# Kernel tuning notes

Measured on AMD Instinct MI355X. Metric: run time of the kernel, lower is better.

Reference implementation:

```python
import jax, jax.numpy as jnp
import numpy as np

N_ATOMS = 200000
AEV_DIM = 384
H1, H2, H3 = 160, 128, 96
N_SPECIES = 4
ALPHA = 0.1  # CELU alpha used by ANI atomic networks


def setup_inputs() -> dict:
    key = jax.random.key(0)
    ks = jax.random.split(key, 8)
    aev = jax.random.normal(ks[0], (N_ATOMS, AEV_DIM), dtype=jnp.float32)
    # Disjoint species partition (matches (species==s).nonzero() buffers)
    perm = jax.random.permutation(ks[1], N_ATOMS)
    chunk = N_ATOMS // N_SPECIES
    H_idx = perm[0 * chunk:1 * chunk]
    C_idx = perm[1 * chunk:2 * chunk]
    N_idx = perm[2 * chunk:3 * chunk]
    O_idx = perm[3 * chunk:4 * chunk]

    def init(k, shape, fan_in):
        return (jax.random.normal(k, shape, dtype=jnp.float32) / np.float32(np.sqrt(fan_in)))

    # Stacked per-species MLP params: leading axis = species (H,C,N,O)
    W1 = init(ks[2], (N_SPECIES, AEV_DIM, H1), AEV_DIM); b1 = jnp.zeros((N_SPECIES, H1), jnp.float32)
    W2 = init(ks[3], (N_SPECIES, H1, H2), H1);          b2 = jnp.zeros((N_SPECIES, H2), jnp.float32)
    W3 = init(ks[4], (N_SPECIES, H2, H3), H2);          b3 = jnp.zeros((N_SPECIES, H3), jnp.float32)
    W4 = init(ks[5], (N_SPECIES, H3, 1), H3);           b4 = jnp.zeros((N_SPECIES, 1), jnp.float32)
    return {"aev": aev,
            "W1": W1, "b1": b1, "W2": W2, "b2": b2,
            "W3": W3, "b3": b3, "W4": W4, "b4": b4,
            "H_idx": H_idx, "C_idx": C_idx, "N_idx": N_idx, "O_idx": O_idx}


def _species_mlp(x, W1, b1, W2, b2, W3, b3, W4, b4):
    h = jax.nn.celu(x @ W1 + b1, ALPHA)
    h = jax.nn.celu(h @ W2 + b2, ALPHA)
    h = jax.nn.celu(h @ W3 + b3, ALPHA)
    return (h @ W4 + b4).reshape(-1)  # per-atom scalar energy


def reference(aev, W1, b1, W2, b2, W3, b3, W4, b4, H_idx, C_idx, N_idx, O_idx):
    out = jnp.zeros((aev.shape[0],), dtype=aev.dtype)
    # Fixed small loop over the 4 species networks (structurally distinct experts)
    for s, idx in enumerate((H_idx, C_idx, N_idx, O_idx)):
        e = _species_mlp(aev[idx], W1[s], b1[s], W2[s], b2[s], W3[s], b3[s], W4[s], b4[s])
        out = out.at[idx].add(e)  # index_add_ scatter
    # output.unsqueeze(0).sum(dim=1) -> molecular energy, shape [1]
    return out[None, :].sum(axis=1)
```

## Files before the change

kernel.cpp:

```cpp
#include <hip/hip_runtime.h>

#define DI __device__ __forceinline__

constexpr int AEV = 384;
constexpr int H1N = 160;
constexpr int H2N = 128;
constexpr int H3N = 96;
constexpr int NSP = 4;
constexpr int W1P = 200;
constexpr int W2P = 168;
constexpr int W3P = 136;
constexpr int W3OFF = H2N * W2P;

using half8  = __attribute__((ext_vector_type(8))) _Float16;
using half4v = __attribute__((ext_vector_type(4))) _Float16;
using f32x4  = __attribute__((ext_vector_type(4))) float;

__device__ __align__(16) _Float16 g_w1[NSP * H1N * AEV];
__device__ __align__(16) _Float16 g_w2[NSP * H2N * H1N];
__device__ __align__(16) _Float16 g_w3[NSP * H3N * H2N];

DI float celu_f(float x) {
  return fmaxf(x, 0.f) + 0.1f * (exp2f(fminf(x, 0.f) * 14.426950408889634f) - 1.f);
}
DI f32x4 mfma16h(half8 a, half8 b, f32x4 c) {
  return __builtin_amdgcn_mfma_f32_16x16x32_f16(a, b, c, 0, 0, 0);
}
DI half8 cvt8(f32x4 a, f32x4 b) {
  half8 t;
  t[0] = (_Float16)a[0]; t[1] = (_Float16)a[1]; t[2] = (_Float16)a[2]; t[3] = (_Float16)a[3];
  t[4] = (_Float16)b[0]; t[5] = (_Float16)b[1]; t[6] = (_Float16)b[2]; t[7] = (_Float16)b[3];
  return t;
}
DI half4v shfl4(half4v v, int src) {
  union { half4v h; int i[2]; } u;
  u.h = v;
  u.i[0] = __shfl(u.i[0], src, 64);
  u.i[1] = __shfl(u.i[1], src, 64);
  return u.h;
}
DI half8 bfrag(const half4v* hb, int ks, int l15, int quad) {
  const int sLo = (quad & 1) * 32 + l15, sHi = sLo + 16;
  half4v loA = shfl4(hb[2 * ks], sLo),     loB = shfl4(hb[2 * ks + 1], sLo);
  half4v hiA = shfl4(hb[2 * ks], sHi),     hiB = shfl4(hb[2 * ks + 1], sHi);
  half4v lo = (quad & 2) ? loB : loA;
  half4v hi = (quad & 2) ? hiB : hiA;
  half8 b;
  b[0] = lo[0]; b[1] = lo[1]; b[2] = lo[2]; b[3] = lo[3];
  b[4] = hi[0]; b[5] = hi[1]; b[6] = hi[2]; b[7] = hi[3];
  return b;
}
DI f32x4 ntl4(const float* p) { return __builtin_nontemporal_load((const f32x4*)p); }

template <int K, int N>
DI void tp(const float* __restrict__ src, _Float16* dst, int id) {
  constexpr int per = K * N;
  int s = id / per, r = id % per;
  int n = r / K, k = r % K;
  dst[s * per + n * K + k] = (_Float16)src[s * per + k * N + n];
}

__global__ void prep(const float* __restrict__ W1, const float* __restrict__ W2,
                     const float* __restrict__ W3, float* __restrict__ out) {
  int id = blockIdx.x * 256 + threadIdx.x;
  if (id == 0) out[0] = 0.f;
  constexpr int E1 = NSP * AEV * H1N;
  constexpr int E2 = NSP * H1N * H2N;
  constexpr int E3 = NSP * H2N * H3N;
  if (id < E1)                 tp<AEV, H1N>(W1, g_w1, id);
  else if (id < E1 + E2)       tp<H1N, H2N>(W2, g_w2, id - E1);
  else if (id < E1 + E2 + E3)  tp<H2N, H3N>(W3, g_w3, id - E1 - E2);
}

__global__ __launch_bounds__(512, 4) void fused_mlp(
    const float* __restrict__ aev,
    const float* __restrict__ b1, const float* __restrict__ b2,
    const float* __restrict__ b3,
    const float* __restrict__ W4, const float* __restrict__ pb4,
    const int* __restrict__ i0, const int* __restrict__ i1,
    const int* __restrict__ i2, const int* __restrict__ i3,
    int chunk, float* __restrict__ out) {
  __shared__ __align__(16) _Float16 WS[34560];
  __shared__ float RED[8];

  const int tid  = threadIdx.x;
  const int lane = tid & 63, wav = tid >> 6;
  const int l15  = lane & 15, quad = lane >> 4;
  const int s    = blockIdx.y;
  const int* idx = (s == 0) ? i0 : (s == 1) ? i1 : (s == 2) ? i2 : i3;

  const int a = blockIdx.x * 128 + wav * 16 + l15;
  const bool valid = (a < chunk);
  const int r = idx[valid ? a : (chunk - 1)];
  const float* xr = aev + (size_t)r * AEV + quad * 8;

  const _Float16* w1src = g_w1 + (size_t)s * H1N * AEV;

#pragma unroll
  for (int i = 0; i < 8; ++i) {
    int c = tid + i * 512;
    if (c < H1N * 24) {
      int n = c / 24, kc = c % 24;
      *(half8*)(WS + n * W1P + kc * 8) = *(const half8*)(w1src + n * AEV + kc * 8);
    }
  }
  __syncthreads();

  f32x4 acc[10];
#pragma unroll
  for (int m = 0; m < 10; ++m)
#pragma unroll
    for (int i = 0; i < 4; ++i) acc[m][i] = 0.f;

  f32x4 xf0 = ntl4(xr), xf1 = ntl4(xr + 4);
#pragma unroll
  for (int ks = 0; ks < 6; ++ks) {
    half8 bv = cvt8(xf0, xf1);
    xf0 = ntl4(xr + (ks + 1) * 32);
    xf1 = ntl4(xr + (ks + 1) * 32 + 4);
#pragma unroll
    for (int mt = 0; mt < 10; ++mt) {
      half8 aw = *(const half8*)(WS + (mt * 16 + l15) * W1P + ks * 32 + quad * 8);
      acc[mt] = mfma16h(aw, bv, acc[mt]);
    }
  }
  __syncthreads();
#pragma unroll
  for (int i = 0; i < 8; ++i) {
    int c = tid + i * 512;
    if (c < H1N * 24) {
      int n = c / 24, kc = c % 24;
      *(half8*)(WS + n * W1P + kc * 8) = *(const half8*)(w1src + 192 + n * AEV + kc * 8);
    }
  }
  __syncthreads();
#pragma unroll
  for (int ks = 6; ks < 12; ++ks) {
    half8 bv = cvt8(xf0, xf1);
    if (ks < 11) {
      xf0 = ntl4(xr + (ks + 1) * 32);
      xf1 = ntl4(xr + (ks + 1) * 32 + 4);
    }
#pragma unroll
    for (int mt = 0; mt < 10; ++mt) {
      half8 aw = *(const half8*)(WS + (mt * 16 + l15) * W1P + (ks - 6) * 32 + quad * 8);
      acc[mt] = mfma16h(aw, bv, acc[mt]);
    }
  }
  half4v hb[10];
#pragma unroll
  for (int mt = 0; mt < 10; ++mt) {
    float4 bb = *(const float4*)(b1 + s * H1N + mt * 16 + quad * 4);
    half4v o;
    o[0] = (_Float16)celu_f(acc[mt][0] + bb.x);
    o[1] = (_Float16)celu_f(acc[mt][1] + bb.y);
    o[2] = (_Float16)celu_f(acc[mt][2] + bb.z);
    o[3] = (_Float16)celu_f(acc[mt][3] + bb.w);
    hb[mt] = o;
  }

  const _Float16* w2src = g_w2 + (size_t)s * H2N * H1N;
  const _Float16* w3src = g_w3 + (size_t)s * H3N * H2N;
  half8 sW0 = *(const half8*)(w2src + (tid / 20) * H1N + (tid % 20) * 8);
  half8 sW1 = *(const half8*)(w2src + ((tid + 512) / 20) * H1N + ((tid + 512) % 20) * 8);
  half8 sW2 = *(const half8*)(w2src + ((tid + 1024) / 20) * H1N + ((tid + 1024) % 20) * 8);
  half8 sW3 = *(const half8*)(w2src + ((tid + 1536) / 20) * H1N + ((tid + 1536) % 20) * 8);
  half8 sW4 = *(const half8*)(w2src + ((tid + 2048) / 20) * H1N + ((tid + 2048) % 20) * 8);
  half8 sV0 = *(const half8*)(w3src + (tid / 16) * H2N + (tid % 16) * 8);
  half8 sV1 = *(const half8*)(w3src + ((tid + 512) / 16) * H2N + ((tid + 512) % 16) * 8);
  half8 sV2 = *(const half8*)(w3src + ((tid + 1024) / 16) * H2N + ((tid + 1024) % 16) * 8);

  __syncthreads();
  *(half8*)(WS + (tid / 20) * W2P + (tid % 20) * 8) = sW0;
  *(half8*)(WS + ((tid + 512) / 20) * W2P + ((tid + 512) % 20) * 8) = sW1;
  *(half8*)(WS + ((tid + 1024) / 20) * W2P + ((tid + 1024) % 20) * 8) = sW2;
  *(half8*)(WS + ((tid + 1536) / 20) * W2P + ((tid + 1536) % 20) * 8) = sW3;
  *(half8*)(WS + ((tid + 2048) / 20) * W2P + ((tid + 2048) % 20) * 8) = sW4;
  *(half8*)(WS + W3OFF + (tid / 16) * W3P + (tid % 16) * 8) = sV0;
  *(half8*)(WS + W3OFF + ((tid + 512) / 16) * W3P + ((tid + 512) % 16) * 8) = sV1;
  *(half8*)(WS + W3OFF + ((tid + 1024) / 16) * W3P + ((tid + 1024) % 16) * 8) = sV2;
  __syncthreads();

  f32x4 acc2[8];
#pragma unroll
  for (int m = 0; m < 8; ++m)
#pragma unroll
    for (int i = 0; i < 4; ++i) acc2[m][i] = 0.f;
#pragma unroll
  for (int ks = 0; ks < 5; ++ks) {
    half8 bv = bfrag(hb, ks, l15, quad);
#pragma unroll
    for (int mt = 0; mt < 8; ++mt) {
      half8 aw = *(const half8*)(WS + (mt * 16 + l15) * W2P + ks * 32 + quad * 8);
      acc2[mt] = mfma16h(aw, bv, acc2[mt]);
    }
  }
  half4v hb2[8];
#pragma unroll
  for (int mt = 0; mt < 8; ++mt) {
    float4 bb = *(const float4*)(b2 + s * H2N + mt * 16 + quad * 4);
    half4v o;
    o[0] = (_Float16)celu_f(acc2[mt][0] + bb.x);
    o[1] = (_Float16)celu_f(acc2[mt][1] + bb.y);
    o[2] = (_Float16)celu_f(acc2[mt][2] + bb.z);
    o[3] = (_Float16)celu_f(acc2[mt][3] + bb.w);
    hb2[mt] = o;
  }

  f32x4 acc3[6];
#pragma unroll
  for (int m = 0; m < 6; ++m)
#pragma unroll
    for (int i = 0; i < 4; ++i) acc3[m][i] = 0.f;
#pragma unroll
  for (int ks = 0; ks < 4; ++ks) {
    half8 bv = bfrag(hb2, ks, l15, quad);
#pragma unroll
    for (int mt = 0; mt < 6; ++mt) {
      half8 aw = *(const half8*)(WS + W3OFF + (mt * 16 + l15) * W3P + ks * 32 + quad * 8);
      acc3[mt] = mfma16h(aw, bv, acc3[mt]);
    }
  }

  float e = 0.f;
#pragma unroll
  for (int mt = 0; mt < 6; ++mt) {
    float4 bb = *(const float4*)(b3 + s * H3N + mt * 16 + quad * 4);
    float4 wv = *(const float4*)(W4 + s * H3N + mt * 16 + quad * 4);
    e += (float)(_Float16)celu_f(acc3[mt][0] + bb.x) * wv.x
       + (float)(_Float16)celu_f(acc3[mt][1] + bb.y) * wv.y
       + (float)(_Float16)celu_f(acc3[mt][2] + bb.z) * wv.z
       + (float)(_Float16)celu_f(acc3[mt][3] + bb.w) * wv.w;
  }
  e += __shfl_xor(e, 16, 64);
  e += __shfl_xor(e, 32, 64);
  e = (lane < 16 && valid) ? (e + pb4[s]) : 0.f;
#pragma unroll
  for (int off = 1; off < 64; off <<= 1) e += __shfl_xor(e, off, 64);
  if (lane == 0) RED[wav] = e;
  __syncthreads();
  if (tid == 0) {
    float t = 0.f;
#pragma unroll
    for (int i = 0; i < 8; ++i) t += RED[i];
    atomicAdd(out, t);
  }
}

extern "C" void kernel_launch(void* const* d_in, const int* in_sizes, int n_in,
                              void* d_out, int out_size, void* d_ws, size_t ws_size,
                              hipStream_t stream) {
  (void)n_in; (void)d_ws; (void)ws_size; (void)out_size;
  const float* aev = (const float*)d_in[0];
  const float* W1  = (const float*)d_in[1];
  const float* b1  = (const float*)d_in[2];
  const float* W2  = (const float*)d_in[3];
  const float* b2  = (const float*)d_in[4];
  const float* W3  = (const float*)d_in[5];
  const float* b3  = (const float*)d_in[6];
  const float* W4  = (const float*)d_in[7];
  const float* b4  = (const float*)d_in[8];
  const int* iH = (const int*)d_in[9];
  const int* iC = (const int*)d_in[10];
  const int* iN = (const int*)d_in[11];
  const int* iO = (const int*)d_in[12];
  const int chunk = in_sizes[9];

  constexpr int TOT = NSP * (AEV * H1N + H1N * H2N + H2N * H3N);
  prep<<<TOT / 256, 256, 0, stream>>>(W1, W2, W3, (float*)d_out);

  const int tiles = (chunk + 127) / 128;
  fused_mlp<<<dim3(tiles, NSP), 512, 0, stream>>>(aev, b1, b2, b3, W4, b4,
                                                  iH, iC, iN, iO, chunk, (float*)d_out);
}
```

Baseline: 472.5 us.

## Make fused MLP persistent with atomic tile queue and prefetch next tile

Replaces the one-block-per-tile grid with 512 persistent blocks, each bound to one species and pulling tiles from a per-species atomic counter reset in the prep kernel. Inside the loop, the next tile's AEV rows and the first W1 half are prefetched while layers 2 and 3 compute, and block partial sums are accumulated locally so there is one global atomic per block. The aim is to hide global load latency and amortize launch and tail overhead. It adds register pressure from the prefetch buffers, may lower occupancy, and relies on the counters being reset before each launch.

```diff
diff --git a/kernel.cpp b/kernel.cpp
--- a/kernel.cpp
+++ b/kernel.cpp
@@ -19,6 +19,7 @@
 __device__ __align__(16) _Float16 g_w1[NSP * H1N * AEV];
 __device__ __align__(16) _Float16 g_w2[NSP * H2N * H1N];
 __device__ __align__(16) _Float16 g_w3[NSP * H3N * H2N];
+__device__ int g_tick[NSP];
 
 DI float celu_f(float x) {
   return fmaxf(x, 0.f) + 0.1f * (exp2f(fminf(x, 0.f) * 14.426950408889634f) - 1.f);
@@ -64,6 +65,7 @@
                      const float* __restrict__ W3, float* __restrict__ out) {
   int id = blockIdx.x * 256 + threadIdx.x;
   if (id == 0) out[0] = 0.f;
+  if (id < NSP) g_tick[id] = 0;
   constexpr int E1 = NSP * AEV * H1N;
   constexpr int E2 = NSP * H1N * H2N;
   constexpr int E3 = NSP * H2N * H3N;
@@ -71,6 +73,13 @@
   else if (id < E1 + E2)       tp<H1N, H2N>(W2, g_w2, id - E1);
   else if (id < E1 + E2 + E3)  tp<H2N, H3N>(W3, g_w3, id - E1 - E2);
 }
+
+#define L1BODY(LK)                                                              \
+  _Pragma("unroll")                                                             \
+  for (int mt = 0; mt < 10; ++mt) {                                             \
+    half8 aw = *(const half8*)(WS + (mt * 16 + l15) * W1P + (LK) * 32 + quad * 8); \
+    acc[mt] = mfma16h(aw, bv, acc[mt]);                                         \
+  }
 
 __global__ __launch_bounds__(512, 4) void fused_mlp(
     const float* __restrict__ aev,
@@ -82,19 +91,38 @@
     int chunk, float* __restrict__ out) {
   __shared__ __align__(16) _Float16 WS[34560];
   __shared__ float RED[8];
+  __shared__ int SHN;
 
   const int tid  = threadIdx.x;
   const int lane = tid & 63, wav = tid >> 6;
   const int l15  = lane & 15, quad = lane >> 4;
-  const int s    = blockIdx.y;
+
+  const int bid = blockIdx.x;
+  const int s   = (bid & 7) >> 1;
   const int* idx = (s == 0) ? i0 : (s == 1) ? i1 : (s == 2) ? i2 : i3;
-
-  const int a = blockIdx.x * 128 + wav * 16 + l15;
-  const bool valid = (a < chunk);
-  const int r = idx[valid ? a : (chunk - 1)];
-  const float* xr = aev + (size_t)r * AEV + quad * 8;
+  const int ntsp = (chunk + 127) >> 7;
 
   const _Float16* w1src = g_w1 + (size_t)s * H1N * AEV;
+  const _Float16* w2src = g_w2 + (size_t)s * H2N * H1N;
+  const _Float16* w3src = g_w3 + (size_t)s * H3N * H2N;
+
+  if (tid == 0) SHN = atomicAdd(&g_tick[s], 1);
+  __syncthreads();
+  int t = SHN;
+  if (t >= ntsp) return;
+
+  bool valid;
+  const float* xr;
+  {
+    int a = t * 128 + wav * 16 + l15;
+    valid = (a < chunk);
+    int r = idx[valid ? a : (chunk - 1)];
+    xr = aev + (size_t)r * AEV + quad * 8;
+  }
+  f32x4 x0a = ntl4(xr),      x0b = ntl4(xr + 4);
+  f32x4 x1a = ntl4(xr + 32), x1b = ntl4(xr + 36);
+  f32x4 x2a = ntl4(xr + 64), x2b = ntl4(xr + 68);
+  f32x4 x3a = ntl4(xr + 96), x3b = ntl4(xr + 100);
 
 #pragma unroll
   for (int i = 0; i < 8; ++i) {
@@ -104,147 +132,176 @@
       *(half8*)(WS + n * W1P + kc * 8) = *(const half8*)(w1src + n * AEV + kc * 8);
     }
   }
+  float bsum = 0.f;
   __syncthreads();
 
-  f32x4 acc[10];
-#pragma unroll
-  for (int m = 0; m < 10; ++m)
-#pragma unroll
-    for (int i = 0; i < 4; ++i) acc[m][i] = 0.f;
-
-  f32x4 xf0 = ntl4(xr), xf1 = ntl4(xr + 4);
-#pragma unroll
-  for (int ks = 0; ks < 6; ++ks) {
-    half8 bv = cvt8(xf0, xf1);
-    xf0 = ntl4(xr + (ks + 1) * 32);
-    xf1 = ntl4(xr + (ks + 1) * 32 + 4);
+  for (;;) {
+    f32x4 acc[10];
+#pragma unroll
+    for (int m = 0; m < 10; ++m)
+#pragma unroll
+      for (int i = 0; i < 4; ++i) acc[m][i] = 0.f;
+
+    { half8 bv = cvt8(x0a, x0b); x0a = ntl4(xr + 128); x0b = ntl4(xr + 132); L1BODY(0) }
+    { half8 bv = cvt8(x1a, x1b); x1a = ntl4(xr + 160); x1b = ntl4(xr + 164); L1BODY(1) }
+    { half8 bv = cvt8(x2a, x2b); x2a = ntl4(xr + 192); x2b = ntl4(xr + 196); L1BODY(2) }
+    { half8 bv = cvt8(x3a, x3b); x3a = ntl4(xr + 224); x3b = ntl4(xr + 228); L1BODY(3) }
+    { half8 bv = cvt8(x0a, x0b); x0a = ntl4(xr + 256); x0b = ntl4(xr + 260); L1BODY(4) }
+    { half8 bv = cvt8(x1a, x1b); x1a = ntl4(xr + 288); x1b = ntl4(xr + 292); L1BODY(5) }
+    __syncthreads();
+#pragma unroll
+    for (int i = 0; i < 8; ++i) {
+      int c = tid + i * 512;
+      if (c < H1N * 24) {
+        int n = c / 24, kc = c % 24;
+        *(half8*)(WS + n * W1P + kc * 8) = *(const half8*)(w1src + 192 + n * AEV + kc * 8);
+      }
+    }
+    __syncthreads();
+    if (tid == 0) SHN = atomicAdd(&g_tick[s], 1);
+
+    { half8 bv = cvt8(x2a, x2b); x2a = ntl4(xr + 320); x2b = ntl4(xr + 324); L1BODY(0) }
+    { half8 bv = cvt8(x3a, x3b); x3a = ntl4(xr + 352); x3b = ntl4(xr + 356); L1BODY(1) }
+    { half8 bv = cvt8(x0a, x0b); L1BODY(2) }
+    { half8 bv = cvt8(x1a, x1b); L1BODY(3) }
+    { half8 bv = cvt8(x2a, x2b); L1BODY(4) }
+    { half8 bv = cvt8(x3a, x3b); L1BODY(5) }
+
+    half4v hb[10];
 #pragma unroll
     for (int mt = 0; mt < 10; ++mt) {
-      half8 aw = *(const half8*)(WS + (mt * 16 + l15) * W1P + ks * 32 + quad * 8);
-      acc[mt] = mfma16h(aw, bv, acc[mt]);
-    }
+      float4 bb = *(const float4*)(b1 + s * H1N + mt * 16 + quad * 4);
+      half4v o;
+      o[0] = (_Float16)celu_f(acc[mt][0] + bb.x);
+      o[1] = (_Float16)celu_f(acc[mt][1] + bb.y);
+      o[2] = (_Float16)celu_f(acc[mt][2] + bb.z);
+      o[3] = (_Float16)celu_f(acc[mt][3] + bb.w);
+      hb[mt] = o;
+    }
+
+    half8 sW0 = *(const half8*)(w2src + (tid / 20) * H1N + (tid % 20) * 8);
+    half8 sW1 = *(const half8*)(w2src + ((tid + 512) / 20) * H1N + ((tid + 512) % 20) * 8);
+    half8 sW2 = *(const half8*)(w2src + ((tid + 1024) / 20) * H1N + ((tid + 1024) % 20) * 8);
+    half8 sW3 = *(const half8*)(w2src + ((tid + 1536) / 20) * H1N + ((tid + 1536) % 20) * 8);
+    half8 sW4 = *(const half8*)(w2src + ((tid + 2048) / 20) * H1N + ((tid + 2048) % 20) * 8);
+    half8 sV0 = *(const half8*)(w3src + (tid / 16) * H2N + (tid % 16) * 8);
+    half8 sV1 = *(const half8*)(w3src + ((tid + 512) / 16) * H2N + ((tid + 512) % 16) * 8);
+    half8 sV2 = *(const half8*)(w3src + ((tid + 1024) / 16) * H2N + ((tid + 1024) % 16) * 8);
+
+    __syncthreads();
+    *(half8*)(WS + (tid / 20) * W2P + (tid % 20) * 8) = sW0;
+    *(half8*)(WS + ((tid + 512) / 20) * W2P + ((tid + 512) % 20) * 8) = sW1;
+    *(half8*)(WS + ((tid + 1024) / 20) * W2P + ((tid + 1024) % 20) * 8) = sW2;
+    *(half8*)(WS + ((tid + 1536) / 20) * W2P + ((tid + 1536) % 20) * 8) = sW3;
+    *(half8*)(WS + ((tid + 2048) / 20) * W2P + ((tid + 2048) % 20) * 8) = sW4;
+    *(half8*)(WS + W3OFF + (tid / 16) * W3P + (tid % 16) * 8) = sV0;
+    *(half8*)(WS + W3OFF + ((tid + 512) / 16) * W3P + ((tid + 512) % 16) * 8) = sV1;
+    *(half8*)(WS + W3OFF + ((tid + 1024) / 16) * W3P + ((tid + 1024) % 16) * 8) = sV2;
+    __syncthreads();
+
+    const int tn = SHN;
+    bool v2;
+    const float* xr2;
+    {
+      int a2 = tn * 128 + wav * 16 + l15;
+      v2 = (tn < ntsp) && (a2 < chunk);
+      int r2 = idx[v2 ? a2 : (chunk - 1)];
+      xr2 = aev + (size_t)r2 * AEV + quad * 8;
+    }
+    x0a = ntl4(xr2);      x0b = ntl4(xr2 + 4);
+    x1a = ntl4(xr2 + 32); x1b = ntl4(xr2 + 36);
+
+    f32x4 acc2[8];
+#pragma unroll
+    for (int m = 0; m < 8; ++m)
+#pragma unroll
+      for (int i = 0; i < 4; ++i) acc2[m][i] = 0.f;
+#pragma unroll
+    for (int ks = 0; ks < 5; ++ks) {
+      half8 bv = bfrag(hb, ks, l15, quad);
+#pragma unroll
+      for (int mt = 0; mt < 8; ++mt) {
+        half8 aw = *(const half8*)(WS + (mt * 16 + l15) * W2P + ks * 32 + quad * 8);
+        acc2[mt] = mfma16h(aw, bv, acc2[mt]);
+      }
+    }
+    half4v hb2[8];
+#pragma unroll
+    for (int mt = 0; mt < 8; ++mt) {
+      float4 bb = *(const float4*)(b2 + s * H2N + mt * 16 + quad * 4);
+      half4v o;
+      o[0] = (_Float16)celu_f(acc2[mt][0] + bb.x);
+      o[1] = (_Float16)celu_f(acc2[mt][1] + bb.y);
+      o[2] = (_Float16)celu_f(acc2[mt][2] + bb.z);
+      o[3] = (_Float16)celu_f(acc2[mt][3] + bb.w);
+      hb2[mt] = o;
+    }
+    x2a = ntl4(xr2 + 64); x2b = ntl4(xr2 + 68);
+    x3a = ntl4(xr2 + 96); x3b = ntl4(xr2 + 100);
+
+    f32x4 acc3[6];
+#pragma unroll
+    for (int m = 0; m < 6; ++m)
+#pragma unroll
+      for (int i = 0; i < 4; ++i) acc3[m][i] = 0.f;
+#pragma unroll
+    for (int ks = 0; ks < 4; ++ks) {
+      half8 bv = bfrag(hb2, ks, l15, quad);
+#pragma unroll
+      for (int mt = 0; mt < 6; ++mt) {
+        half8 aw = *(const half8*)(WS + W3OFF + (mt * 16 + l15) * W3P + ks * 32 + quad * 8);
+        acc3[mt] = mfma16h(aw, bv, acc3[mt]);
+      }
+    }
+
+    half8 sH[8];
+#pragma unroll
+    for (int i = 0; i < 8; ++i) {
+      int c = tid + i * 512;
+      if (c < H1N * 24) {
+        int n = c / 24, kc = c % 24;
+        sH[i] = *(const half8*)(w1src + n * AEV + kc * 8);
+      }
+    }
+
+    float e = 0.f;
+#pragma unroll
+    for (int mt = 0; mt < 6; ++mt) {
+      float4 bb = *(const float4*)(b3 + s * H3N + mt * 16 + quad * 4);
+      float4 wv = *(const float4*)(W4 + s * H3N + mt * 16 + quad * 4);
+      e += (float)(_Float16)celu_f(acc3[mt][0] + bb.x) * wv.x
+         + (float)(_Float16)celu_f(acc3[mt][1] + bb.y) * wv.y
+         + (float)(_Float16)celu_f(acc3[mt][2] + bb.z) * wv.z
+         + (float)(_Float16)celu_f(acc3[mt][3] + bb.w) * wv.w;
+    }
+    e += __shfl_xor(e, 16, 64);
+    e += __shfl_xor(e, 32, 64);
+    e = (lane < 16 && valid) ? (e + pb4[s]) : 0.f;
+#pragma unroll
+    for (int off = 1; off < 64; off <<= 1) e += __shfl_xor(e, off, 64);
+    if (lane == 0) RED[wav] = e;
+    __syncthreads();
+    if (tid == 0) {
+      float ts = 0.f;
+#pragma unroll
+      for (int i = 0; i < 8; ++i) ts += RED[i];
+      bsum += ts;
+    }
+    if (tn >= ntsp) break;
+
+#pragma unroll
+    for (int i = 0; i < 8; ++i) {
+      int c = tid + i * 512;
+      if (c < H1N * 24) {
+        int n = c / 24, kc = c % 24;
+        *(half8*)(WS + n * W1P + kc * 8) = sH[i];
+      }
+    }
+    valid = v2;
+    xr = xr2;
+    __syncthreads();
   }
-  __syncthreads();
-#pragma unroll
-  for (int i = 0; i < 8; ++i) {
-    int c = tid + i * 512;
-    if (c < H1N * 24) {
-      int n = c / 24, kc = c % 24;
-      *(half8*)(WS + n * W1P + kc * 8) = *(const half8*)(w1src + 192 + n * AEV + kc * 8);
-    }
-  }
-  __syncthreads();
-#pragma unroll
-  for (int ks = 6; ks < 12; ++ks) {
-    half8 bv = cvt8(xf0, xf1);
-    if (ks < 11) {
-      xf0 = ntl4(xr + (ks + 1) * 32);
-      xf1 = ntl4(xr + (ks + 1) * 32 + 4);
-    }
-#pragma unroll
-    for (int mt = 0; mt < 10; ++mt) {
-      half8 aw = *(const half8*)(WS + (mt * 16 + l15) * W1P + (ks - 6) * 32 + quad * 8);
-      acc[mt] = mfma16h(aw, bv, acc[mt]);
-    }
-  }
-  half4v hb[10];
-#pragma unroll
-  for (int mt = 0; mt < 10; ++mt) {
-    float4 bb = *(const float4*)(b1 + s * H1N + mt * 16 + quad * 4);
-    half4v o;
-    o[0] = (_Float16)celu_f(acc[mt][0] + bb.x);
-    o[1] = (_Float16)celu_f(acc[mt][1] + bb.y);
-    o[2] = (_Float16)celu_f(acc[mt][2] + bb.z);
-    o[3] = (_Float16)celu_f(acc[mt][3] + bb.w);
-    hb[mt] = o;
-  }
-
-  const _Float16* w2src = g_w2 + (size_t)s * H2N * H1N;
-  const _Float16* w3src = g_w3 + (size_t)s * H3N * H2N;
-  half8 sW0 = *(const half8*)(w2src + (tid / 20) * H1N + (tid % 20) * 8);
-  half8 sW1 = *(const half8*)(w2src + ((tid + 512) / 20) * H1N + ((tid + 512) % 20) * 8);
-  half8 sW2 = *(const half8*)(w2src + ((tid + 1024) / 20) * H1N + ((tid + 1024) % 20) * 8);
-  half8 sW3 = *(const half8*)(w2src + ((tid + 1536) / 20) * H1N + ((tid + 1536) % 20) * 8);
-  half8 sW4 = *(const half8*)(w2src + ((tid + 2048) / 20) * H1N + ((tid + 2048) % 20) * 8);
-  half8 sV0 = *(const half8*)(w3src + (tid / 16) * H2N + (tid % 16) * 8);
-  half8 sV1 = *(const half8*)(w3src + ((tid + 512) / 16) * H2N + ((tid + 512) % 16) * 8);
-  half8 sV2 = *(const half8*)(w3src + ((tid + 1024) / 16) * H2N + ((tid + 1024) % 16) * 8);
-
-  __syncthreads();
-  *(half8*)(WS + (tid / 20) * W2P + (tid % 20) * 8) = sW0;
-  *(half8*)(WS + ((tid + 512) / 20) * W2P + ((tid + 512) % 20) * 8) = sW1;
-  *(half8*)(WS + ((tid + 1024) / 20) * W2P + ((tid + 1024) % 20) * 8) = sW2;
-  *(half8*)(WS + ((tid + 1536) / 20) * W2P + ((tid + 1536) % 20) * 8) = sW3;
-  *(half8*)(WS + ((tid + 2048) / 20) * W2P + ((tid + 2048) % 20) * 8) = sW4;
-  *(half8*)(WS + W3OFF + (tid / 16) * W3P + (tid % 16) * 8) = sV0;
-  *(half8*)(WS + W3OFF + ((tid + 512) / 16) * W3P + ((tid + 512) % 16) * 8) = sV1;
-  *(half8*)(WS + W3OFF + ((tid + 1024) / 16) * W3P + ((tid + 1024) % 16) * 8) = sV2;
-  __syncthreads();
-
-  f32x4 acc2[8];
-#pragma unroll
-  for (int m = 0; m < 8; ++m)
-#pragma unroll
-    for (int i = 0; i < 4; ++i) acc2[m][i] = 0.f;
-#pragma unroll
-  for (int ks = 0; ks < 5; ++ks) {
-    half8 bv = bfrag(hb, ks, l15, quad);
-#pragma unroll
-    for (int mt = 0; mt < 8; ++mt) {
-      half8 aw = *(const half8*)(WS + (mt * 16 + l15) * W2P + ks * 32 + quad * 8);
-      acc2[mt] = mfma16h(aw, bv, acc2[mt]);
-    }
-  }
-  half4v hb2[8];
-#pragma unroll
-  for (int mt = 0; mt < 8; ++mt) {
-    float4 bb = *(const float4*)(b2 + s * H2N + mt * 16 + quad * 4);
-    half4v o;
-    o[0] = (_Float16)celu_f(acc2[mt][0] + bb.x);
-    o[1] = (_Float16)celu_f(acc2[mt][1] + bb.y);
-    o[2] = (_Float16)celu_f(acc2[mt][2] + bb.z);
-    o[3] = (_Float16)celu_f(acc2[mt][3] + bb.w);
-    hb2[mt] = o;
-  }
-
-  f32x4 acc3[6];
-#pragma unroll
-  for (int m = 0; m < 6; ++m)
-#pragma unroll
-    for (int i = 0; i < 4; ++i) acc3[m][i] = 0.f;
-#pragma unroll
-  for (int ks = 0; ks < 4; ++ks) {
-    half8 bv = bfrag(hb2, ks, l15, quad);
-#pragma unroll
-    for (int mt = 0; mt < 6; ++mt) {
-      half8 aw = *(const half8*)(WS + W3OFF + (mt * 16 + l15) * W3P + ks * 32 + quad * 8);
-      acc3[mt] = mfma16h(aw, bv, acc3[mt]);
-    }
-  }
-
-  float e = 0.f;
-#pragma unroll
-  for (int mt = 0; mt < 6; ++mt) {
-    float4 bb = *(const float4*)(b3 + s * H3N + mt * 16 + quad * 4);
-    float4 wv = *(const float4*)(W4 + s * H3N + mt * 16 + quad * 4);
-    e += (float)(_Float16)celu_f(acc3[mt][0] + bb.x) * wv.x
-       + (float)(_Float16)celu_f(acc3[mt][1] + bb.y) * wv.y
-       + (float)(_Float16)celu_f(acc3[mt][2] + bb.z) * wv.z
-       + (float)(_Float16)celu_f(acc3[mt][3] + bb.w) * wv.w;
-  }
-  e += __shfl_xor(e, 16, 64);
-  e += __shfl_xor(e, 32, 64);
-  e = (lane < 16 && valid) ? (e + pb4[s]) : 0.f;
-#pragma unroll
-  for (int off = 1; off < 64; off <<= 1) e += __shfl_xor(e, off, 64);
-  if (lane == 0) RED[wav] = e;
-  __syncthreads();
-  if (tid == 0) {
-    float t = 0.f;
-#pragma unroll
-    for (int i = 0; i < 8; ++i) t += RED[i];
-    atomicAdd(out, t);
-  }
+  if (tid == 0) atomicAdd(out, bsum);
 }
 
 extern "C" void kernel_launch(void* const* d_in, const int* in_sizes, int n_in,
@@ -269,7 +326,6 @@
   constexpr int TOT = NSP * (AEV * H1N + H1N * H2N + H2N * H3N);
   prep<<<TOT / 256, 256, 0, stream>>>(W1, W2, W3, (float*)d_out);
 
-  const int tiles = (chunk + 127) / 128;
-  fused_mlp<<<dim3(tiles, NSP), 512, 0, stream>>>(aev, b1, b2, b3, W4, b4,
-                                                  iH, iC, iN, iO, chunk, (float*)d_out);
-}
+  fused_mlp<<<dim3(512), 512, 0, stream>>>(aev, b1, b2, b3, W4, b4,
+                                           iH, iC, iN, iO, chunk, (float*)d_out);
+}
```

Result: slower. 596.8 us (+26.3%).
